# Kernel optimization log

Measured on AMD Instinct MI355X. Metric: run time of the kernel, lower is better.

The kernel has to match this reference:

```python
import jax, jax.numpy as jnp
import numpy as np

D_MODEL = 768
N_HEADS = 12
D_HEAD = 64
WINDOW = 16
LOOK_BACK = 1
IGNORE = -1.0e6


def look_around(x, backward=LOOK_BACK, forward=0, pad_value=0):
    # x: (b, n_windows, w, ...) -> (b, n_windows, w*(backward+forward+1), ...)
    n = x.shape[1]
    pad = [(0, 0)] * x.ndim
    pad[1] = (backward, forward)
    px = jnp.pad(x, pad, constant_values=pad_value)
    return jnp.concatenate([px[:, i:i + n] for i in range(backward + forward + 1)], axis=2)


def setup_inputs() -> dict:
    key = jax.random.key(0)
    k1, k2, k3 = jax.random.split(key, 3)
    B, T = 2, 2048
    x = jax.random.normal(k1, (B, T, D_MODEL), dtype=jnp.float32)
    W_abcde = jax.random.normal(k2, (D_MODEL, 5 * N_HEADS * D_HEAD), dtype=jnp.float32) * (1.0 / np.sqrt(D_MODEL))
    b_abcde = jnp.zeros((5 * N_HEADS * D_HEAD,), dtype=jnp.float32)
    W_O = jax.random.normal(k3, (N_HEADS * D_HEAD, D_MODEL), dtype=jnp.float32) * (1.0 / np.sqrt(N_HEADS * D_HEAD))
    b_O = jnp.zeros((D_MODEL,), dtype=jnp.float32)
    return {"x": x, "W_abcde": W_abcde, "b_abcde": b_abcde, "W_O": W_O, "b_O": b_O}


def reference(x, W_abcde, b_abcde, W_O, b_O):
    B, T, _ = x.shape
    w = WINDOW
    nw = T // w
    Ww = w * (LOOK_BACK + 1)  # look-around window length

    abcde = x @ W_abcde + b_abcde                                    # (B,T,5*H*D)
    abcde = abcde.reshape(B, T, 5, N_HEADS, D_HEAD).transpose(2, 0, 3, 1, 4)  # (5,B,H,T,D)
    a, b, c, d, e = [t.reshape(B * N_HEADS, nw, w, D_HEAD) for t in abcde]
    a_l, b_l, d_l, e_l = (look_around(t) for t in (a, b, d, e))       # (BH,nw,Ww,D)

    # causal mask, same construction as get_causal_mask (pad_value=0)
    seq = jnp.arange(T).reshape(1, nw, w)
    bb = look_around(seq)                                            # (1,nw,Ww)
    # mask[n,m,l] = (seq_n < bb_l) | (bb_l <= bb_m)
    mask = (seq[..., :, None, None] < bb[..., None, None, :]) | (bb[..., None, None, :] <= bb[..., None, :, None])

    # third-order attention scores: (BH, nw, w, Ww, Ww)
    scores = jnp.einsum('bnwd,bnmd,bnld->bnwml', c, a_l, b_l)
    scores = jnp.where(mask, IGNORE, scores)
    scores = jnp.where(scores == 0, IGNORE, scores)
    probs = jax.nn.softmax((scores / D_HEAD).reshape(B * N_HEADS, nw, w, Ww * Ww), axis=-1)
    probs = probs.reshape(scores.shape)

    z = jnp.einsum('bnwml,bnmd->bnwd', probs, d_l) + jnp.einsum('bnwml,bnld->bnwd', probs, e_l)
    z = z.reshape(B, N_HEADS, nw, w, D_HEAD).transpose(0, 2, 3, 1, 4).reshape(B, T, N_HEADS * D_HEAD)
    return z @ W_O + b_O
```

## Files before the change

### kernel.cpp

```cpp
#include <hip/hip_runtime.h>

#define T_SEQ   2048
#define NHEADS  12
#define DHEAD   64
#define WIN     16
#define WW      32
#define NWIN    128
#define DMODEL  768
#define NABCDE  3840
#define IGNORE_V (-1.0e6f)
#define PAD_K   72
#define L2E64   0.022542110013890053f

typedef float f32x4 __attribute__((ext_vector_type(4)));
typedef float f32x2 __attribute__((ext_vector_type(2)));
typedef short bf16x8 __attribute__((ext_vector_type(8)));

__device__ __forceinline__ short f2bf(float f) {
    unsigned u = __float_as_uint(f);
    unsigned r = (u + 0x7FFF + ((u >> 16) & 1)) >> 16;
    return (short)r;
}

__device__ __forceinline__ void gload_lds16(const short* g, short* l) {
    __builtin_amdgcn_global_load_lds(
        (const __attribute__((address_space(1))) void*)g,
        (__attribute__((address_space(3))) void*)l,
        16, 0, 0);
}

__global__ __launch_bounds__(256) void prep_kernel(
    const float* __restrict__ x, const float* __restrict__ W_abcde,
    const float* __restrict__ W_O,
    short* __restrict__ xb, short* __restrict__ Wt, short* __restrict__ WOt)
{
    __shared__ float tile[32][33];
    const int blk = blockIdx.x;
    const int tid = threadIdx.x;

    if (blk < 1536) {
        int i = (blk * 256 + tid) * 8;
        float4 a = *reinterpret_cast<const float4*>(&x[i]);
        float4 b = *reinterpret_cast<const float4*>(&x[i + 4]);
        union { short s[8]; uint4 u; } r;
        r.s[0] = f2bf(a.x); r.s[1] = f2bf(a.y); r.s[2] = f2bf(a.z); r.s[3] = f2bf(a.w);
        r.s[4] = f2bf(b.x); r.s[5] = f2bf(b.y); r.s[6] = f2bf(b.z); r.s[7] = f2bf(b.w);
        *reinterpret_cast<uint4*>(&xb[i]) = r.u;
        return;
    }
    const float* W; short* Wo; int N, bx, by;
    if (blk < 4416) {
        int t = blk - 1536;
        W = W_abcde; Wo = Wt; N = NABCDE;
        bx = (t % 120) * 32; by = (t / 120) * 32;
    } else {
        int t = blk - 4416;
        W = W_O; Wo = WOt; N = DMODEL;
        bx = (t % 24) * 32; by = (t / 24) * 32;
    }
    const int tx = tid & 31, ty = tid >> 5;
#pragma unroll
    for (int r = 0; r < 32; r += 8)
        tile[ty + r][tx] = W[(size_t)(by + ty + r) * N + bx + tx];
    __syncthreads();
#pragma unroll
    for (int r = 0; r < 32; r += 8)
        Wo[(size_t)(bx + ty + r) * DMODEL + by + tx] = f2bf(tile[tx][ty + r]);
}

__global__ __launch_bounds__(256) void gemm1_kernel(
    const short* __restrict__ A, const short* __restrict__ Bt,
    const float* __restrict__ bias, short* __restrict__ C,
    int M, int N, int K)
{
    __shared__ short As[2][128 * 32];
    __shared__ short Bs[2][64 * 32];

    const int tid  = threadIdx.x;
    const int wave = tid >> 6;
    const int lane = tid & 63;

    int bid = blockIdx.x;
    int xcd = bid & 7, t = bid >> 3;
    int sid = (t / 80) * 8 + xcd;
    int inner = t % 80;
    int sy = sid / 6, sn = sid - sy * 6;
    const int bm = (sy * 8 + (inner & 7)) * 128;
    const int bn = (sn * 10 + (inner >> 3)) * 64;

    const int st_row = lane >> 2;
    const int st_col = (lane & 3) * 8;
    const int fr_m = lane & 15;
    const int fr_k = (lane >> 4) * 8;
    const int wm = wave * 32;
    const int lc = lane & 15;
    const int ko = lane >> 4;

    const short* gsrc[6];
    short* ldst[6];
#pragma unroll
    for (int j = 0; j < 6; ++j) {
        int c = wave * 6 + j;
        if (c < 16) {
            int kt = c >> 3, rg = c & 7;
            gsrc[j] = A + (size_t)(bm + rg * 16 + st_row) * K + kt * 32 + st_col;
            ldst[j] = &As[kt][(rg * 16) * 32];
        } else {
            int cb = c - 16;
            int kt = cb >> 2, rg = cb & 3;
            gsrc[j] = Bt + (size_t)(bn + rg * 16 + st_row) * K + kt * 32 + st_col;
            ldst[j] = &Bs[kt][(rg * 16) * 32];
        }
    }

    f32x4 acc[2][4];
#pragma unroll
    for (int mi = 0; mi < 2; ++mi)
#pragma unroll
        for (int ni = 0; ni < 4; ++ni) acc[mi][ni] = (f32x4){0.f, 0.f, 0.f, 0.f};

    for (int k0 = 0; k0 < K; k0 += 64) {
#pragma unroll
        for (int j = 0; j < 6; ++j) gload_lds16(gsrc[j] + k0, ldst[j]);
        __syncthreads();

#pragma unroll
        for (int kt = 0; kt < 2; ++kt) {
            bf16x8 af[2], bf[4];
#pragma unroll
            for (int mi = 0; mi < 2; ++mi)
                af[mi] = *reinterpret_cast<const bf16x8*>(
                    &As[kt][(wm + mi * 16 + fr_m) * 32 + fr_k]);
#pragma unroll
            for (int ni = 0; ni < 4; ++ni)
                bf[ni] = *reinterpret_cast<const bf16x8*>(
                    &Bs[kt][(ni * 16 + fr_m) * 32 + fr_k]);
#pragma unroll
            for (int mi = 0; mi < 2; ++mi)
#pragma unroll
                for (int ni = 0; ni < 4; ++ni)
                    acc[mi][ni] = __builtin_amdgcn_mfma_f32_16x16x32_bf16(
                        af[mi], bf[ni], acc[mi][ni], 0, 0, 0);
        }
        __syncthreads();
    }

    float bv[4];
#pragma unroll
    for (int ni = 0; ni < 4; ++ni)
        bv[ni] = bias[bn + ni * 16 + lc];

    short* cb = &As[0][0];
#pragma unroll
    for (int mi = 0; mi < 2; ++mi) {
#pragma unroll
        for (int r = 0; r < 4; ++r) {
            int row = wm + mi * 16 + ko * 4 + r;
#pragma unroll
            for (int ni = 0; ni < 4; ++ni)
                cb[row * 64 + ni * 16 + lc] = f2bf(acc[mi][ni][r] + bv[ni]);
        }
    }
    __syncthreads();
#pragma unroll
    for (int q = 0; q < 4; ++q) {
        int f = tid + q * 256;
        int row = f >> 3, c16 = (f & 7) * 8;
        *reinterpret_cast<uint4*>(&C[(size_t)(bm + row) * N + bn + c16]) =
            *reinterpret_cast<const uint4*>(&cb[row * 64 + c16]);
    }
}

__global__ __launch_bounds__(256) void gemm_bf16_64(
    const short* __restrict__ A, const short* __restrict__ Bt,
    const float* __restrict__ bias, float* __restrict__ C,
    int M, int N, int K)
{
    __shared__ short As[2][64 * 32];
    __shared__ short Bs[2][64 * 32];

    const int tid  = threadIdx.x;
    const int wave = tid >> 6;
    const int lane = tid & 63;
    const int bm = blockIdx.y * 64;
    const int bn = blockIdx.x * 64;

    const int st_row = lane >> 2;
    const int st_col = (lane & 3) * 8;
    const int fr_m = lane & 15;
    const int fr_k = (lane >> 4) * 8;
    const int wm = wave * 16;

    const short* gsrc[4];
    short* ldst[4];
#pragma unroll
    for (int j = 0; j < 4; ++j) {
        int c = wave * 4 + j;
        if (c < 8) {
            int kt = c >> 2, rg = c & 3;
            gsrc[j] = A + (size_t)(bm + rg * 16 + st_row) * K + kt * 32 + st_col;
            ldst[j] = &As[kt][(rg * 16) * 32];
        } else {
            int cb = c - 8;
            int kt = cb >> 2, rg = cb & 3;
            gsrc[j] = Bt + (size_t)(bn + rg * 16 + st_row) * K + kt * 32 + st_col;
            ldst[j] = &Bs[kt][(rg * 16) * 32];
        }
    }

    f32x4 acc[4];
#pragma unroll
    for (int ni = 0; ni < 4; ++ni) acc[ni] = (f32x4){0.f, 0.f, 0.f, 0.f};

    for (int k0 = 0; k0 < K; k0 += 64) {
#pragma unroll
        for (int j = 0; j < 4; ++j) gload_lds16(gsrc[j] + k0, ldst[j]);
        __syncthreads();

#pragma unroll
        for (int kt = 0; kt < 2; ++kt) {
            bf16x8 af = *reinterpret_cast<const bf16x8*>(
                &As[kt][(wm + fr_m) * 32 + fr_k]);
#pragma unroll
            for (int ni = 0; ni < 4; ++ni) {
                bf16x8 bf = *reinterpret_cast<const bf16x8*>(
                    &Bs[kt][(ni * 16 + fr_m) * 32 + fr_k]);
                acc[ni] = __builtin_amdgcn_mfma_f32_16x16x32_bf16(
                    af, bf, acc[ni], 0, 0, 0);
            }
        }
        __syncthreads();
    }

    float bv[4];
#pragma unroll
    for (int ni = 0; ni < 4; ++ni)
        bv[ni] = bias[bn + ni * 16 + (lane & 15)];
    int rbase = bm + wm + (lane >> 4) * 4;
#pragma unroll
    for (int r = 0; r < 4; ++r) {
        size_t off = (size_t)(rbase + r) * N + bn + (lane & 15);
#pragma unroll
        for (int ni = 0; ni < 4; ++ni)
            C[off + ni * 16] = acc[ni][r] + bv[ni];
    }
}

__global__ __launch_bounds__(256) void attn_kernel(
    const short* __restrict__ abcde, short* __restrict__ z)
{
    const int blk = blockIdx.x;
    const int n  = blk & (NWIN - 1);
    const int bh = blk >> 7;
    const int b  = bh / NHEADS;
    const int h  = bh % NHEADS;

    __shared__ short sc[WIN * PAD_K];
    __shared__ short sa[WW * PAD_K];
    __shared__ short sb[WW * PAD_K];
    __shared__ short sd[WW * PAD_K];
    __shared__ short se[WW * PAD_K];
    __shared__ short epA[WIN * PAD_K];
    __shared__ float sinv[WIN];

    const int tid = threadIdx.x;
    const size_t rowbase = ((size_t)b * T_SEQ) * NABCDE;
    const int hd = h * DHEAD;

    if (tid < 128) {
        int row = tid >> 3, ch = (tid & 7) * 8;
        *reinterpret_cast<uint4*>(&sc[row * PAD_K + ch]) =
            *reinterpret_cast<const uint4*>(
                &abcde[rowbase + (size_t)(n * WIN + row) * NABCDE + 2 * DMODEL + hd + ch]);
    }
    {
        int row = tid >> 3, ch = (tid & 7) * 8;
        int t = n * WIN - WIN + row;
        uint4 va = {0u, 0u, 0u, 0u}, vb = va, vd = va, ve = va;
        if (t >= 0) {
            size_t base = rowbase + (size_t)t * NABCDE + hd + ch;
            va = *reinterpret_cast<const uint4*>(&abcde[base + 0 * DMODEL]);
            vb = *reinterpret_cast<const uint4*>(&abcde[base + 1 * DMODEL]);
            vd = *reinterpret_cast<const uint4*>(&abcde[base + 3 * DMODEL]);
            ve = *reinterpret_cast<const uint4*>(&abcde[base + 4 * DMODEL]);
        }
        *reinterpret_cast<uint4*>(&sa[row * PAD_K + ch]) = va;
        *reinterpret_cast<uint4*>(&sb[row * PAD_K + ch]) = vb;
        *reinterpret_cast<uint4*>(&sd[row * PAD_K + ch]) = vd;
        *reinterpret_cast<uint4*>(&se[row * PAD_K + ch]) = ve;
    }
    __syncthreads();

    const int wv = tid >> 6;
    const int lane = tid & 63;
    const int lc = lane & 15;
    const int ko = lane >> 4;

    f32x2 c2[2][4];
    bf16x8 bfrag[2][2];
#pragma unroll
    for (int kt = 0; kt < 2; ++kt) {
        union { bf16x8 v; unsigned u[4]; } Cf;
        Cf.v = *reinterpret_cast<const bf16x8*>(
            &sc[(wv * 4 + (lc & 3)) * PAD_K + kt * 32 + ko * 8]);
#pragma unroll
        for (int j = 0; j < 4; ++j) {
            c2[kt][j] = (f32x2){__uint_as_float(Cf.u[j] << 16),
                                __uint_as_float(Cf.u[j] & 0xffff0000u)};
        }
        bfrag[0][kt] = *reinterpret_cast<const bf16x8*>(&sb[lc * PAD_K + kt * 32 + ko * 8]);
        bfrag[1][kt] = *reinterpret_cast<const bf16x8*>(&sb[(16 + lc) * PAD_K + kt * 32 + ko * 8]);
    }

    f32x4 acc[8][2];
#pragma unroll
    for (int mt = 0; mt < 8; ++mt) {
        acc[mt][0] = (f32x4){0.f, 0.f, 0.f, 0.f};
        acc[mt][1] = (f32x4){0.f, 0.f, 0.f, 0.f};
    }
#pragma unroll
    for (int mt = 0; mt < 8; ++mt) {
#pragma unroll
        for (int kt = 0; kt < 2; ++kt) {
            union { bf16x8 v; unsigned u[4]; } Ar, Rf;
            Ar.v = *reinterpret_cast<const bf16x8*>(
                &sa[(mt * 4 + (lc >> 2)) * PAD_K + kt * 32 + ko * 8]);
#pragma unroll
            for (int j = 0; j < 4; ++j) {
                f32x2 y = (f32x2){__uint_as_float(Ar.u[j] << 16),
                                  __uint_as_float(Ar.u[j] & 0xffff0000u)};
                f32x2 p = c2[kt][j] * y;
                Rf.u[j] = __builtin_amdgcn_perm(
                    __float_as_uint(p[1]), __float_as_uint(p[0]), 0x07060302);
            }
            acc[mt][0] = __builtin_amdgcn_mfma_f32_16x16x32_bf16(Rf.v, bfrag[0][kt], acc[mt][0], 0, 0, 0);
            acc[mt][1] = __builtin_amdgcn_mfma_f32_16x16x32_bf16(Rf.v, bfrag[1][kt], acc[mt][1], 0, 0, 0);
        }
    }

    const int nbase = n * WIN;
    int bbl_h[2];
    bool keepL[2][4];
#pragma unroll
    for (int lt = 0; lt < 2; ++lt) {
        int l = lt * 16 + lc;
        bbl_h[lt] = (n == 0 && l < WIN) ? 0 : (nbase - WIN + l);
#pragma unroll
        for (int reg = 0; reg < 4; ++reg)
            keepL[lt][reg] = (nbase + wv * 4 + reg) >= bbl_h[lt];
    }
#pragma unroll
    for (int mt = 0; mt < 8; ++mt) {
        int m = mt * 4 + ko;
        int bbm = (n == 0 && m < WIN) ? 0 : (nbase - WIN + m);
#pragma unroll
        for (int lt = 0; lt < 2; ++lt) {
            bool mgt = bbl_h[lt] > bbm;
#pragma unroll
            for (int reg = 0; reg < 4; ++reg) {
                if (!(keepL[lt][reg] && mgt)) acc[mt][lt][reg] = IGNORE_V;
            }
        }
    }
    if (n == 0) {
#pragma unroll
        for (int mt = 0; mt < 8; ++mt)
#pragma unroll
            for (int lt = 0; lt < 2; ++lt)
#pragma unroll
                for (int reg = 0; reg < 4; ++reg)
                    if (acc[mt][lt][reg] == 0.0f) acc[mt][lt][reg] = IGNORE_V;
    }

    float mx[4] = {-3.4e38f, -3.4e38f, -3.4e38f, -3.4e38f};
#pragma unroll
    for (int mt = 0; mt < 8; ++mt)
#pragma unroll
        for (int lt = 0; lt < 2; ++lt)
#pragma unroll
            for (int reg = 0; reg < 4; ++reg)
                mx[reg] = fmaxf(mx[reg], acc[mt][lt][reg]);
#pragma unroll
    for (int reg = 0; reg < 4; ++reg) {
#pragma unroll
        for (int off = 1; off < 64; off <<= 1)
            mx[reg] = fmaxf(mx[reg], __shfl_xor(mx[reg], off, 64));
    }

    float c0[4];
#pragma unroll
    for (int reg = 0; reg < 4; ++reg) c0[reg] = -mx[reg] * L2E64;
#pragma unroll
    for (int mt = 0; mt < 8; ++mt)
#pragma unroll
        for (int lt = 0; lt < 2; ++lt)
#pragma unroll
            for (int reg = 0; reg < 4; ++reg)
                acc[mt][lt][reg] = exp2f(fmaf(acc[mt][lt][reg], L2E64, c0[reg]));

    float plv[2][4];
#pragma unroll
    for (int lt = 0; lt < 2; ++lt) {
#pragma unroll
        for (int reg = 0; reg < 4; ++reg) {
            float p = acc[0][lt][reg];
#pragma unroll
            for (int mt = 1; mt < 8; ++mt) p += acc[mt][lt][reg];
            p += __shfl_xor(p, 16, 64);
            p += __shfl_xor(p, 32, 64);
            plv[lt][reg] = p;
        }
        float w  = (ko & 1) ? plv[lt][1] : plv[lt][0];
        float w2 = (ko & 1) ? plv[lt][3] : plv[lt][2];
        float ww = (ko & 2) ? w2 : w;
        epA[(wv * 4 + ko) * PAD_K + 32 + lt * 16 + lc] = f2bf(ww);
    }

    {
        float s[4];
#pragma unroll
        for (int reg = 0; reg < 4; ++reg) {
            float t = plv[0][reg] + plv[1][reg];
            t += __shfl_xor(t, 1, 64);
            t += __shfl_xor(t, 2, 64);
            t += __shfl_xor(t, 4, 64);
            t += __shfl_xor(t, 8, 64);
            s[reg] = t;
        }
        if (lane == 0) {
#pragma unroll
            for (int reg = 0; reg < 4; ++reg) sinv[wv * 4 + reg] = 1.0f / s[reg];
        }
    }

    {
        float v8[8][4];
#pragma unroll
        for (int mt = 0; mt < 8; ++mt)
#pragma unroll
            for (int reg = 0; reg < 4; ++reg)
                v8[mt][reg] = acc[mt][0][reg] + acc[mt][1][reg];

        const bool s0 = lane & 1, s1 = lane & 2, s2 = lane & 4, s3 = lane & 8;
        float r1[4][4];
#pragma unroll
        for (int m2 = 0; m2 < 4; ++m2)
#pragma unroll
            for (int reg = 0; reg < 4; ++reg) {
                float u = v8[2 * m2][reg], w = v8[2 * m2 + 1][reg];
                float a = s0 ? w : u;
                float s = s0 ? u : w;
                r1[m2][reg] = a + __shfl_xor(s, 1, 64);
            }
        float r2[2][4];
#pragma unroll
        for (int m4 = 0; m4 < 2; ++m4)
#pragma unroll
            for (int reg = 0; reg < 4; ++reg) {
                float u = r1[2 * m4][reg], w = r1[2 * m4 + 1][reg];
                float a = s1 ? w : u;
                float s = s1 ? u : w;
                r2[m4][reg] = a + __shfl_xor(s, 2, 64);
            }
        float r3[4];
#pragma unroll
        for (int reg = 0; reg < 4; ++reg) {
            float u = r2[0][reg], w = r2[1][reg];
            float a = s2 ? w : u;
            float s = s2 ? u : w;
            r3[reg] = a + __shfl_xor(s, 4, 64);
        }
        float a0 = s3 ? r3[1] : r3[0];
        float q0 = s3 ? r3[0] : r3[1];
        float g0 = a0 + __shfl_xor(q0, 8, 64);
        float a1 = s3 ? r3[3] : r3[2];
        float q1 = s3 ? r3[2] : r3[3];
        float g1 = a1 + __shfl_xor(q1, 8, 64);

        int mcol = (lc & 7) * 4 + ko;
        int ib = wv * 4 + (lc >> 3);
        epA[ib * PAD_K + mcol]       = f2bf(g0);
        epA[(ib + 2) * PAD_K + mcol] = f2bf(g1);
    }

    const int dd = wv * 16 + lc;
    bf16x8 bd, be;
    {
        unsigned dv[8], ev[8];
#pragma unroll
        for (int j = 0; j < 8; ++j) {
            dv[j] = *reinterpret_cast<const unsigned short*>(&sd[(ko * 8 + j) * PAD_K + dd]);
            ev[j] = *reinterpret_cast<const unsigned short*>(&se[(ko * 8 + j) * PAD_K + dd]);
        }
        union { unsigned u[4]; bf16x8 v; } td, te;
#pragma unroll
        for (int j = 0; j < 4; ++j) {
            td.u[j] = __builtin_amdgcn_perm(dv[2 * j + 1], dv[2 * j], 0x05040100);
            te.u[j] = __builtin_amdgcn_perm(ev[2 * j + 1], ev[2 * j], 0x05040100);
        }
        bd = td.v; be = te.v;
    }
    __syncthreads();

    bf16x8 apm = *reinterpret_cast<const bf16x8*>(&epA[lc * PAD_K + ko * 8]);
    bf16x8 apl = *reinterpret_cast<const bf16x8*>(&epA[lc * PAD_K + 32 + ko * 8]);
    f32x4 zacc = (f32x4){0.f, 0.f, 0.f, 0.f};
    zacc = __builtin_amdgcn_mfma_f32_16x16x32_bf16(apm, bd, zacc, 0, 0, 0);
    zacc = __builtin_amdgcn_mfma_f32_16x16x32_bf16(apl, be, zacc, 0, 0, 0);

    short* zs = sd;
#pragma unroll
    for (int reg = 0; reg < 4; ++reg) {
        int i = ko * 4 + reg;
        zs[i * 64 + dd] = f2bf(zacc[reg] * sinv[i]);
    }
    __syncthreads();
    {
        int row = tid >> 4;
        int ch  = (tid & 15) * 4;
        *reinterpret_cast<uint2*>(
            &z[((size_t)b * T_SEQ + nbase + row) * (NHEADS * DHEAD) + hd + ch]) =
            *reinterpret_cast<const uint2*>(&zs[row * 64 + ch]);
    }
}

extern "C" void kernel_launch(void* const* d_in, const int* in_sizes, int n_in,
                              void* d_out, int out_size, void* d_ws, size_t ws_size,
                              hipStream_t stream) {
    const float* x        = (const float*)d_in[0];
    const float* W_abcde  = (const float*)d_in[1];
    const float* b_abcde  = (const float*)d_in[2];
    const float* W_O      = (const float*)d_in[3];
    const float* b_O      = (const float*)d_in[4];
    float* out = (float*)d_out;

    char* ws = (char*)d_ws;
    short* abcde = (short*)ws;
    short* xb    = (short*)(ws + (size_t)31457280);
    short* Wt    = (short*)(ws + (size_t)31457280 + 6291456);
    short* WOt   = (short*)(ws + (size_t)31457280 + 6291456 + 5898240);
    short* zb    = xb;

    const int M = 2 * T_SEQ;

    prep_kernel<<<dim3(4992), dim3(256), 0, stream>>>(
        x, W_abcde, W_O, xb, Wt, WOt);

    gemm1_kernel<<<dim3(1920), dim3(256), 0, stream>>>(
        xb, Wt, b_abcde, abcde, M, NABCDE, DMODEL);

    attn_kernel<<<dim3(2 * NHEADS * NWIN), dim3(256), 0, stream>>>(abcde, zb);

    gemm_bf16_64<<<dim3(DMODEL / 64, M / 64), dim3(256), 0, stream>>>(
        zb, WOt, b_O, out, M, DMODEL, DMODEL);
}
```

Baseline: 169.2 us.

## Enlarge QKV GEMM tiles to 128x128 and use 128x64 tiles for output GEMM

The first projection GEMM now computes 128x128 output tiles per block, with each wave holding a 64x64 accumulator set, and launches half as many blocks. Its epilogue stages results through LDS in two halves. The output GEMM is replaced by a 128x64-tile kernel that also remaps blocks across XCDs. Larger tiles raise arithmetic intensity and cut redundant global loads, at the cost of more registers, fewer blocks in flight, and extra barriers in the epilogue.

```diff
diff --git a/kernel.cpp b/kernel.cpp
--- a/kernel.cpp
+++ b/kernel.cpp
@@ -74,7 +74,7 @@
     int M, int N, int K)
 {
     __shared__ short As[2][128 * 32];
-    __shared__ short Bs[2][64 * 32];
+    __shared__ short Bs[2][128 * 32];
 
     const int tid  = threadIdx.x;
     const int wave = tid >> 6;
@@ -82,11 +82,122 @@
 
     int bid = blockIdx.x;
     int xcd = bid & 7, t = bid >> 3;
-    int sid = (t / 80) * 8 + xcd;
-    int inner = t % 80;
-    int sy = sid / 6, sn = sid - sy * 6;
-    const int bm = (sy * 8 + (inner & 7)) * 128;
-    const int bn = (sn * 10 + (inner >> 3)) * 64;
+    int sidx = t / 40, inner = t % 40;
+    int sid = sidx * 8 + xcd;
+    int sy = sid / 3, sx = sid % 3;
+    const int ty = sy * 4 + (inner & 3);
+    const int tx = sx * 10 + (inner >> 2);
+    const int bm = ty * 128;
+    const int bn = tx * 128;
+
+    const int st_row = lane >> 2;
+    const int st_col = (lane & 3) * 8;
+    const int fr_m = lane & 15;
+    const int fr_k = (lane >> 4) * 8;
+    const int ko   = lane >> 4;
+    const int wr = wave >> 1;
+    const int wm = wr * 64;
+    const int wn = (wave & 1) * 64;
+
+    const short* gsrc[8];
+    short* ldst[8];
+#pragma unroll
+    for (int j = 0; j < 8; ++j) {
+        int c = wave * 8 + j;
+        if (c < 16) {
+            int kt = c >> 3, rg = c & 7;
+            gsrc[j] = A + (size_t)(bm + rg * 16 + st_row) * K + kt * 32 + st_col;
+            ldst[j] = &As[kt][(rg * 16) * 32];
+        } else {
+            int cb = c - 16;
+            int kt = cb >> 3, rg = cb & 7;
+            gsrc[j] = Bt + (size_t)(bn + rg * 16 + st_row) * K + kt * 32 + st_col;
+            ldst[j] = &Bs[kt][(rg * 16) * 32];
+        }
+    }
+
+    f32x4 acc[4][4];
+#pragma unroll
+    for (int mi = 0; mi < 4; ++mi)
+#pragma unroll
+        for (int ni = 0; ni < 4; ++ni) acc[mi][ni] = (f32x4){0.f, 0.f, 0.f, 0.f};
+
+    for (int k0 = 0; k0 < K; k0 += 64) {
+#pragma unroll
+        for (int j = 0; j < 8; ++j) gload_lds16(gsrc[j] + k0, ldst[j]);
+        __syncthreads();
+
+#pragma unroll
+        for (int kt = 0; kt < 2; ++kt) {
+            bf16x8 af[4], bfv[4];
+#pragma unroll
+            for (int mi = 0; mi < 4; ++mi)
+                af[mi] = *reinterpret_cast<const bf16x8*>(
+                    &As[kt][(wm + mi * 16 + fr_m) * 32 + fr_k]);
+#pragma unroll
+            for (int ni = 0; ni < 4; ++ni)
+                bfv[ni] = *reinterpret_cast<const bf16x8*>(
+                    &Bs[kt][(wn + ni * 16 + fr_m) * 32 + fr_k]);
+#pragma unroll
+            for (int mi = 0; mi < 4; ++mi)
+#pragma unroll
+                for (int ni = 0; ni < 4; ++ni)
+                    acc[mi][ni] = __builtin_amdgcn_mfma_f32_16x16x32_bf16(
+                        af[mi], bfv[ni], acc[mi][ni], 0, 0, 0);
+        }
+        __syncthreads();
+    }
+
+    float bv[4];
+#pragma unroll
+    for (int ni = 0; ni < 4; ++ni)
+        bv[ni] = bias[bn + wn + ni * 16 + fr_m];
+
+    short* cb = &As[0][0];
+#pragma unroll
+    for (int half = 0; half < 2; ++half) {
+        if (wr == half) {
+#pragma unroll
+            for (int mi = 0; mi < 4; ++mi) {
+#pragma unroll
+                for (int r = 0; r < 4; ++r) {
+                    int row = mi * 16 + ko * 4 + r;
+#pragma unroll
+                    for (int ni = 0; ni < 4; ++ni)
+                        cb[row * 128 + wn + ni * 16 + fr_m] =
+                            f2bf(acc[mi][ni][r] + bv[ni]);
+                }
+            }
+        }
+        __syncthreads();
+#pragma unroll
+        for (int q = 0; q < 4; ++q) {
+            int f = tid + q * 256;
+            int row = f >> 4, c16 = (f & 15) * 8;
+            *reinterpret_cast<uint4*>(
+                &C[(size_t)(bm + half * 64 + row) * N + bn + c16]) =
+                *reinterpret_cast<const uint4*>(&cb[row * 128 + c16]);
+        }
+        __syncthreads();
+    }
+}
+
+__global__ __launch_bounds__(256) void gemm2_kernel(
+    const short* __restrict__ A, const short* __restrict__ Bt,
+    const float* __restrict__ bias, float* __restrict__ C,
+    int M, int N, int K)
+{
+    __shared__ short As[2][128 * 32];
+    __shared__ short Bs[2][64 * 32];
+
+    const int tid  = threadIdx.x;
+    const int wave = tid >> 6;
+    const int lane = tid & 63;
+
+    int bid = blockIdx.x;
+    int wgid = (bid & 7) * 48 + (bid >> 3);
+    const int bm = (wgid / 12) * 128;
+    const int bn = (wgid % 12) * 64;
 
     const int st_row = lane >> 2;
     const int st_col = (lane & 3) * 8;
@@ -149,100 +260,16 @@
 #pragma unroll
     for (int ni = 0; ni < 4; ++ni)
         bv[ni] = bias[bn + ni * 16 + lc];
-
-    short* cb = &As[0][0];
+    int rbase = bm + wm + ko * 4;
 #pragma unroll
     for (int mi = 0; mi < 2; ++mi) {
 #pragma unroll
         for (int r = 0; r < 4; ++r) {
-            int row = wm + mi * 16 + ko * 4 + r;
+            size_t off = (size_t)(rbase + mi * 16 + r) * N + bn + lc;
 #pragma unroll
             for (int ni = 0; ni < 4; ++ni)
-                cb[row * 64 + ni * 16 + lc] = f2bf(acc[mi][ni][r] + bv[ni]);
-        }
-    }
-    __syncthreads();
-#pragma unroll
-    for (int q = 0; q < 4; ++q) {
-        int f = tid + q * 256;
-        int row = f >> 3, c16 = (f & 7) * 8;
-        *reinterpret_cast<uint4*>(&C[(size_t)(bm + row) * N + bn + c16]) =
-            *reinterpret_cast<const uint4*>(&cb[row * 64 + c16]);
-    }
-}
-
-__global__ __launch_bounds__(256) void gemm_bf16_64(
-    const short* __restrict__ A, const short* __restrict__ Bt,
-    const float* __restrict__ bias, float* __restrict__ C,
-    int M, int N, int K)
-{
-    __shared__ short As[2][64 * 32];
-    __shared__ short Bs[2][64 * 32];
-
-    const int tid  = threadIdx.x;
-    const int wave = tid >> 6;
-    const int lane = tid & 63;
-    const int bm = blockIdx.y * 64;
-    const int bn = blockIdx.x * 64;
-
-    const int st_row = lane >> 2;
-    const int st_col = (lane & 3) * 8;
-    const int fr_m = lane & 15;
-    const int fr_k = (lane >> 4) * 8;
-    const int wm = wave * 16;
-
-    const short* gsrc[4];
-    short* ldst[4];
-#pragma unroll
-    for (int j = 0; j < 4; ++j) {
-        int c = wave * 4 + j;
-        if (c < 8) {
-            int kt = c >> 2, rg = c & 3;
-            gsrc[j] = A + (size_t)(bm + rg * 16 + st_row) * K + kt * 32 + st_col;
-            ldst[j] = &As[kt][(rg * 16) * 32];
-        } else {
-            int cb = c - 8;
-            int kt = cb >> 2, rg = cb & 3;
-            gsrc[j] = Bt + (size_t)(bn + rg * 16 + st_row) * K + kt * 32 + st_col;
-            ldst[j] = &Bs[kt][(rg * 16) * 32];
-        }
-    }
-
-    f32x4 acc[4];
-#pragma unroll
-    for (int ni = 0; ni < 4; ++ni) acc[ni] = (f32x4){0.f, 0.f, 0.f, 0.f};
-
-    for (int k0 = 0; k0 < K; k0 += 64) {
-#pragma unroll
-        for (int j = 0; j < 4; ++j) gload_lds16(gsrc[j] + k0, ldst[j]);
-        __syncthreads();
-
-#pragma unroll
-        for (int kt = 0; kt < 2; ++kt) {
-            bf16x8 af = *reinterpret_cast<const bf16x8*>(
-                &As[kt][(wm + fr_m) * 32 + fr_k]);
-#pragma unroll
-            for (int ni = 0; ni < 4; ++ni) {
-                bf16x8 bf = *reinterpret_cast<const bf16x8*>(
-                    &Bs[kt][(ni * 16 + fr_m) * 32 + fr_k]);
-                acc[ni] = __builtin_amdgcn_mfma_f32_16x16x32_bf16(
-                    af, bf, acc[ni], 0, 0, 0);
-            }
-        }
-        __syncthreads();
-    }
-
-    float bv[4];
-#pragma unroll
-    for (int ni = 0; ni < 4; ++ni)
-        bv[ni] = bias[bn + ni * 16 + (lane & 15)];
-    int rbase = bm + wm + (lane >> 4) * 4;
-#pragma unroll
-    for (int r = 0; r < 4; ++r) {
-        size_t off = (size_t)(rbase + r) * N + bn + (lane & 15);
-#pragma unroll
-        for (int ni = 0; ni < 4; ++ni)
-            C[off + ni * 16] = acc[ni][r] + bv[ni];
+                C[off + ni * 16] = acc[mi][ni][r] + bv[ni];
+        }
     }
 }
 
@@ -546,11 +573,11 @@
     prep_kernel<<<dim3(4992), dim3(256), 0, stream>>>(
         x, W_abcde, W_O, xb, Wt, WOt);
 
-    gemm1_kernel<<<dim3(1920), dim3(256), 0, stream>>>(
+    gemm1_kernel<<<dim3(960), dim3(256), 0, stream>>>(
         xb, Wt, b_abcde, abcde, M, NABCDE, DMODEL);
 
     attn_kernel<<<dim3(2 * NHEADS * NWIN), dim3(256), 0, stream>>>(abcde, zb);
 
-    gemm_bf16_64<<<dim3(DMODEL / 64, M / 64), dim3(256), 0, stream>>>(
+    gemm2_kernel<<<dim3(384), dim3(256), 0, stream>>>(
         zb, WOt, b_O, out, M, DMODEL, DMODEL);
 }
```

Result: no change. 172.5 us (+1.9%).
